# Optimization experiments

Measured on AMD Instinct MI355X. Metric: run time of the kernel, lower is better.

## Reference

```python
import jax, jax.numpy as jnp
import numpy as np

B, S, E, H = 2, 2048, 1024, 16
D = E // H  # head size

def setup_inputs() -> dict:
    key = jax.random.key(0)
    ks = jax.random.split(key, 11)
    s = 0.02
    return {
        "q": jax.random.normal(ks[0], (B, S, E), jnp.float32),
        "k": jax.random.normal(ks[1], (B, S, E), jnp.float32),
        "v": jax.random.normal(ks[2], (B, S, E), jnp.float32),
        "Wq": jax.random.normal(ks[3], (E, E), jnp.float32) * s,
        "bq": jax.random.normal(ks[4], (E,), jnp.float32) * s,
        "Wk": jax.random.normal(ks[5], (E, E), jnp.float32) * s,
        "bk": jax.random.normal(ks[6], (E,), jnp.float32) * s,
        "Wv": jax.random.normal(ks[7], (E, E), jnp.float32) * s,
        "bv": jax.random.normal(ks[8], (E,), jnp.float32) * s,
        "Wo": jax.random.normal(ks[9], (E, E), jnp.float32) * s,
        "bo": jax.random.normal(ks[10], (E,), jnp.float32) * s,
    }

def reference(q, k, v, Wq, bq, Wk, bk, Wv, bv, Wo, bo):
    b, sq, _ = q.shape
    sk = k.shape[1]
    # linear projections, split into heads: [B,S,H,D]
    qh = (q @ Wq.T + bq).reshape(b, sq, H, D)
    kh = (k @ Wk.T + bk).reshape(b, sk, H, D)
    vh = (v @ Wv.T + bv).reshape(b, sk, H, D)
    # NOTE: original module does NOT scale by 1/sqrt(D)
    scores = jnp.einsum('bqhe,bkhe->bhqk', qh, kh)
    probs = jax.nn.softmax(scores, axis=-1)  # dropout = identity (eval)
    attn = jnp.einsum('bhqk,bkhe->bqhe', probs, vh).reshape(b, sq, E)
    return attn @ Wo.T + bo
```

## Files before the change

kernel.cpp:

```cpp
#include <hip/hip_runtime.h>
#include <stdint.h>

#define BH 2
#define SEQ 2048
#define EMB 1024
#define NH 16
#define HD 64
#define MROWS (BH * SEQ)
#define BHN (BH * NH)
#define LOG2E 1.44269504f

typedef __attribute__((ext_vector_type(8))) short bf16x8;
typedef __attribute__((ext_vector_type(4))) float f32x4;

static __device__ __forceinline__ unsigned short f2bf(float x) {
  union { float f; unsigned int u; } a; a.f = x;
  unsigned int r = a.u + 0x7fffu + ((a.u >> 16) & 1u);
  return (unsigned short)(r >> 16);
}

static __device__ __forceinline__ unsigned int cvtpk(float lo, float hi) {
  unsigned int r;
  asm("v_cvt_pk_bf16_f32 %0, %1, %2" : "=v"(r) : "v"(lo), "v"(hi));
  return r;
}

static __device__ __forceinline__ float vexp2(float x) {
  float r;
  asm("v_exp_f32 %0, %1" : "=v"(r) : "v"(x));
  return r;
}

struct Conv7 { const float* s[7]; unsigned short* d[7]; };

__global__ __launch_bounds__(256) void conv_all(Conv7 a) {
  const int b = blockIdx.x;
  int r, off;
  if (b < 12288) { r = b >> 12; off = b & 4095; }
  else { int t = b - 12288; r = 3 + (t >> 10); off = t & 1023; }
  const int i = (off * 256 + threadIdx.x) * 4;
  float4 v = *(const float4*)(a.s[r] + i);
  ushort4 o;
  o.x = f2bf(v.x); o.y = f2bf(v.y); o.z = f2bf(v.z); o.w = f2bf(v.w);
  *(ushort4*)(a.d[r] + i) = o;
}

struct B3 { const float* p[3]; };
struct Out3 { void* p[3]; };

template <int MODE>
__global__ __launch_bounds__(256) void gemm128(const unsigned short* __restrict__ Abase,
                                               const unsigned short* __restrict__ Bbase,
                                               B3 biases, Out3 outs) {
  __shared__ unsigned short lA[128 * 64];
  __shared__ unsigned short lB[128 * 64];
  const int z = blockIdx.z;
  const unsigned short* A  = Abase + (size_t)z * MROWS * EMB;
  const unsigned short* Bt = Bbase + (size_t)z * EMB * EMB;
  const float* bias = biases.p[z];
  const int tid = threadIdx.x;
  const int lane = tid & 63;
  const int w = tid >> 6;
  const int row0 = blockIdx.x * 128;
  const int col0 = blockIdx.y * 128;
  const int wr = (w >> 1) * 64;
  const int wc = (w & 1) * 64;
  const int r16 = lane & 15;
  const int g = lane >> 4;

  const int s_rowoff = (lane >> 3);
  const int s_col = ((lane & 7) ^ s_rowoff) * 8;

  f32x4 acc[4][4] = {};

  for (int kt = 0; kt < EMB / 64; ++kt) {
    const int k0 = kt * 64;
    __syncthreads();
#pragma unroll
    for (int j = 0; j < 4; ++j) {
      const int chunk = w * 4 + j;
      const int row = chunk * 8 + s_rowoff;
      __builtin_amdgcn_global_load_lds(
          (const __attribute__((address_space(1))) void*)(A + (size_t)(row0 + row) * EMB + k0 + s_col),
          (__attribute__((address_space(3))) void*)(lA + chunk * 512), 16, 0, 0);
      __builtin_amdgcn_global_load_lds(
          (const __attribute__((address_space(1))) void*)(Bt + (size_t)(col0 + row) * EMB + k0 + s_col),
          (__attribute__((address_space(3))) void*)(lB + chunk * 512), 16, 0, 0);
    }
    __syncthreads();
#pragma unroll
    for (int kk = 0; kk < 2; ++kk) {
      bf16x8 a[4], b[4];
#pragma unroll
      for (int m = 0; m < 4; ++m) {
        const int row = wr + m * 16 + r16;
        a[m] = *(const bf16x8*)(lA + row * 64 + (((kk << 2) + g) ^ (r16 & 7)) * 8);
      }
#pragma unroll
      for (int n = 0; n < 4; ++n) {
        const int row = wc + n * 16 + r16;
        b[n] = *(const bf16x8*)(lB + row * 64 + (((kk << 2) + g) ^ (r16 & 7)) * 8);
      }
#pragma unroll
      for (int m = 0; m < 4; ++m)
#pragma unroll
        for (int n = 0; n < 4; ++n)
          acc[m][n] = __builtin_amdgcn_mfma_f32_16x16x32_bf16(a[m], b[n], acc[m][n], 0, 0, 0);
    }
  }

  const float scl = (MODE == 0 && z == 0) ? LOG2E : 1.0f;
#pragma unroll
  for (int m = 0; m < 4; ++m) {
#pragma unroll
    for (int n = 0; n < 4; ++n) {
      const int colg = col0 + wc + n * 16 + r16;
      const float bv = bias[colg];
      const int rowbase = row0 + wr + m * 16 + g * 4;
      if (MODE == 0 && z == 2) {
        const int b_ = rowbase >> 11, s_ = rowbase & 2047;
        const int h_ = colg >> 6, d_ = colg & 63;
        ushort4 pk;
        pk.x = f2bf(acc[m][n][0] + bv);
        pk.y = f2bf(acc[m][n][1] + bv);
        pk.z = f2bf(acc[m][n][2] + bv);
        pk.w = f2bf(acc[m][n][3] + bv);
        *(ushort4*)((unsigned short*)outs.p[2] +
                    ((size_t)(b_ * NH + h_) * HD + d_) * SEQ + s_) = pk;
      } else {
#pragma unroll
        for (int j = 0; j < 4; ++j) {
          const int rowg = rowbase + j;
          const float v = (acc[m][n][j] + bv) * scl;
          if (MODE == 0) {
            const int b_ = rowg >> 11, s_ = rowg & 2047;
            const int h_ = colg >> 6, d_ = colg & 63;
            ((unsigned short*)outs.p[z])
                [(((size_t)(b_ * NH + h_) * SEQ + s_) << 6) + d_] = f2bf(v);
          } else {
            ((float*)outs.p[0])[(size_t)rowg * EMB + colg] = v;
          }
        }
      }
    }
  }
}

__global__ __launch_bounds__(256) void attn_fwd(const unsigned short* __restrict__ Qh,
                                                const unsigned short* __restrict__ Kh,
                                                const unsigned short* __restrict__ Vt,
                                                unsigned short* __restrict__ ctx) {
  __shared__ unsigned short lK[64 * 72];
  __shared__ unsigned short lV[64 * 72];
  __shared__ unsigned short lP[4][2][16 * 72];
  const int tid = threadIdx.x;
  const int lane = tid & 63;
  const int w = tid >> 6;
  const int r16 = lane & 15;
  const int g = lane >> 4;
  const int wg = blockIdx.x;
  const int xcd = wg & 7;
  const int slot = wg >> 3;
  const int bh = xcd + 8 * (slot >> 4);
  const int qb = slot & 15;
  const size_t base = (size_t)bh * SEQ * HD;
  const unsigned short* Q = Qh + base;
  const unsigned short* K = Kh + base;
  const unsigned short* V = Vt + base;
  const int q0 = qb * 128 + w * 32;

  bf16x8 bq[2][2];
#pragma unroll
  for (int mi = 0; mi < 2; ++mi)
#pragma unroll
    for (int kk = 0; kk < 2; ++kk)
      bq[mi][kk] = *(const bf16x8*)(Q + (size_t)(q0 + mi * 16 + r16) * HD + kk * 32 + g * 8);

  f32x4 oacc[2][4] = {};
  float lsum[2] = {0.f, 0.f};

  const int sr = tid >> 2;
  const int sc = (tid & 3) * 16;

  uint4 kr0 = *(const uint4*)(K + (size_t)sr * HD + sc);
  uint4 kr1 = *(const uint4*)(K + (size_t)sr * HD + sc + 8);
  uint4 vr0 = *(const uint4*)(V + (size_t)sr * SEQ + sc);
  uint4 vr1 = *(const uint4*)(V + (size_t)sr * SEQ + sc + 8);

  for (int t = 0; t < SEQ / 64; ++t) {
    __syncthreads();
    *(uint4*)(lK + sr * 72 + sc)     = kr0;
    *(uint4*)(lK + sr * 72 + sc + 8) = kr1;
    *(uint4*)(lV + sr * 72 + sc)     = vr0;
    *(uint4*)(lV + sr * 72 + sc + 8) = vr1;
    __syncthreads();

    if (t < SEQ / 64 - 1) {
      const int kv1 = (t + 1) * 64;
      kr0 = *(const uint4*)(K + (size_t)(kv1 + sr) * HD + sc);
      kr1 = *(const uint4*)(K + (size_t)(kv1 + sr) * HD + sc + 8);
      vr0 = *(const uint4*)(V + (size_t)sr * SEQ + kv1 + sc);
      vr1 = *(const uint4*)(V + (size_t)sr * SEQ + kv1 + sc + 8);
    }

    f32x4 st[2][4] = {};
    __builtin_amdgcn_s_setprio(1);
#pragma unroll
    for (int kk = 0; kk < 2; ++kk) {
      bf16x8 ak[4];
#pragma unroll
      for (int n = 0; n < 4; ++n)
        ak[n] = *(const bf16x8*)(lK + (n * 16 + r16) * 72 + kk * 32 + g * 8);
#pragma unroll
      for (int mi = 0; mi < 2; ++mi)
#pragma unroll
        for (int n = 0; n < 4; ++n)
          st[mi][n] = __builtin_amdgcn_mfma_f32_16x16x32_bf16(ak[n], bq[mi][kk], st[mi][n], 0, 0, 0);
    }
    __builtin_amdgcn_s_setprio(0);

#pragma unroll
    for (int mi = 0; mi < 2; ++mi) {
      float ls = 0.f;
#pragma unroll
      for (int n = 0; n < 4; ++n) {
        float p0 = vexp2(st[mi][n][0]);
        float p1 = vexp2(st[mi][n][1]);
        float p2 = vexp2(st[mi][n][2]);
        float p3 = vexp2(st[mi][n][3]);
        ls += (p0 + p1) + (p2 + p3);
        uint2 pk;
        pk.x = cvtpk(p0, p1);
        pk.y = cvtpk(p2, p3);
        *(uint2*)(&lP[w][mi][r16 * 72 + n * 16 + g * 4]) = pk;
      }
      lsum[mi] += ls;
    }
    asm volatile("s_waitcnt lgkmcnt(0)" ::: "memory");
    __builtin_amdgcn_sched_barrier(0);

    __builtin_amdgcn_s_setprio(1);
#pragma unroll
    for (int kk = 0; kk < 2; ++kk) {
      bf16x8 bv[4];
#pragma unroll
      for (int nd = 0; nd < 4; ++nd)
        bv[nd] = *(const bf16x8*)(lV + (nd * 16 + r16) * 72 + kk * 32 + g * 8);
#pragma unroll
      for (int mi = 0; mi < 2; ++mi) {
        bf16x8 ap = *(const bf16x8*)(&lP[w][mi][r16 * 72 + kk * 32 + g * 8]);
#pragma unroll
        for (int nd = 0; nd < 4; ++nd)
          oacc[mi][nd] = __builtin_amdgcn_mfma_f32_16x16x32_bf16(ap, bv[nd], oacc[mi][nd], 0, 0, 0);
      }
    }
    __builtin_amdgcn_s_setprio(0);
  }

  float linv[2];
#pragma unroll
  for (int mi = 0; mi < 2; ++mi) {
    float v = lsum[mi];
    v += __shfl_xor(v, 16, 64);
    v += __shfl_xor(v, 32, 64);
    linv[mi] = 1.0f / v;
  }
  float rr[2][4];
#pragma unroll
  for (int mi = 0; mi < 2; ++mi)
#pragma unroll
    for (int j = 0; j < 4; ++j)
      rr[mi][j] = __shfl(linv[mi], g * 4 + j, 64);

  const int b_ = bh >> 4, h_ = bh & 15;
#pragma unroll
  for (int mi = 0; mi < 2; ++mi)
#pragma unroll
    for (int nd = 0; nd < 4; ++nd)
#pragma unroll
      for (int j = 0; j < 4; ++j) {
        const int srow = q0 + mi * 16 + g * 4 + j;
        const int col = h_ * 64 + nd * 16 + r16;
        ctx[((size_t)(b_ * SEQ + srow) << 10) + col] = f2bf(oacc[mi][nd][j] * rr[mi][j]);
      }
}

extern "C" void kernel_launch(void* const* d_in, const int* in_sizes, int n_in,
                              void* d_out, int out_size, void* d_ws, size_t ws_size,
                              hipStream_t stream) {
  const float* q  = (const float*)d_in[0];
  const float* k  = (const float*)d_in[1];
  const float* v  = (const float*)d_in[2];
  const float* Wq = (const float*)d_in[3];
  const float* bq = (const float*)d_in[4];
  const float* Wk = (const float*)d_in[5];
  const float* bk = (const float*)d_in[6];
  const float* Wv = (const float*)d_in[7];
  const float* bv = (const float*)d_in[8];
  const float* Wo = (const float*)d_in[9];
  const float* bo = (const float*)d_in[10];

  char* ws = (char*)d_ws;
  const size_t SZ_ACT = (size_t)MROWS * EMB * 2;
  const size_t SZ_W   = (size_t)EMB * EMB * 2;
  unsigned short* qb  = (unsigned short*)(ws);
  unsigned short* kb  = (unsigned short*)(ws + SZ_ACT);
  unsigned short* vb  = (unsigned short*)(ws + 2 * SZ_ACT);
  unsigned short* Wqb = (unsigned short*)(ws + 3 * SZ_ACT);
  unsigned short* Wob = (unsigned short*)(ws + 3 * SZ_ACT + 3 * SZ_W);
  unsigned short* Qh  = (unsigned short*)(ws + 3 * SZ_ACT + 4 * SZ_W);
  unsigned short* Kh  = (unsigned short*)(ws + 4 * SZ_ACT + 4 * SZ_W);
  unsigned short* Vt  = (unsigned short*)(ws + 5 * SZ_ACT + 4 * SZ_W);
  unsigned short* ctx = (unsigned short*)(ws + 6 * SZ_ACT + 4 * SZ_W);

  Conv7 ca;
  ca.s[0] = q;  ca.s[1] = k;  ca.s[2] = v;
  ca.s[3] = Wq; ca.s[4] = Wk; ca.s[5] = Wv; ca.s[6] = Wo;
  ca.d[0] = qb; ca.d[1] = kb; ca.d[2] = vb;
  ca.d[3] = Wqb; ca.d[4] = Wqb + EMB * EMB; ca.d[5] = Wqb + 2 * EMB * EMB; ca.d[6] = Wob;
  conv_all<<<16384, 256, 0, stream>>>(ca);

  B3 bqkv; bqkv.p[0] = bq; bqkv.p[1] = bk; bqkv.p[2] = bv;
  Out3 oqkv; oqkv.p[0] = (void*)Qh; oqkv.p[1] = (void*)Kh; oqkv.p[2] = (void*)Vt;
  gemm128<0><<<dim3(MROWS / 128, EMB / 128, 3), 256, 0, stream>>>(qb, Wqb, bqkv, oqkv);

  attn_fwd<<<512, 256, 0, stream>>>(Qh, Kh, Vt, ctx);

  B3 bout; bout.p[0] = bo; bout.p[1] = bo; bout.p[2] = bo;
  Out3 oout; oout.p[0] = d_out; oout.p[1] = d_out; oout.p[2] = d_out;
  gemm128<1><<<dim3(MROWS / 128, EMB / 128, 1), 256, 0, stream>>>(ctx, Wob, bout, oout);
}
```

Baseline: 238.6 us.

## Rewrite attention with 32x32 MFMA, register P via permlane swap, double-buffered LDS

The attention kernel switches from 16x16x32 to 32x32x16 MFMA tiles. The probability tile is rearranged in registers with v_permlane32_swap, so it no longer round-trips through LDS. K/V tiles are double-buffered in swizzled LDS, which leaves one barrier per iteration instead of two. The QKV projection GEMM epilogue now stages outputs through shared memory to emit coalesced 16-byte stores into the head-major and transposed-V layouts, at the cost of extra barriers and LDS traffic.

Result: faster. 231.0 us (-3.2%).

```diff
diff --git a/kernel.cpp b/kernel.cpp
--- a/kernel.cpp
+++ b/kernel.cpp
@@ -12,6 +12,7 @@
 
 typedef __attribute__((ext_vector_type(8))) short bf16x8;
 typedef __attribute__((ext_vector_type(4))) float f32x4;
+typedef __attribute__((ext_vector_type(16))) float f32x16;
 
 static __device__ __forceinline__ unsigned short f2bf(float x) {
   union { float f; unsigned int u; } a; a.f = x;
@@ -29,6 +30,10 @@
   float r;
   asm("v_exp_f32 %0, %1" : "=v"(r) : "v"(x));
   return r;
+}
+
+static __device__ __forceinline__ void plswap(unsigned int& a, unsigned int& b) {
+  asm volatile("v_permlane32_swap_b32 %0, %1" : "+v"(a), "+v"(b));
 }
 
 struct Conv7 { const float* s[7]; unsigned short* d[7]; };
@@ -52,8 +57,9 @@
 __global__ __launch_bounds__(256) void gemm128(const unsigned short* __restrict__ Abase,
                                                const unsigned short* __restrict__ Bbase,
                                                B3 biases, Out3 outs) {
-  __shared__ unsigned short lA[128 * 64];
-  __shared__ unsigned short lB[128 * 64];
+  __shared__ unsigned short lsm[128 * 128];
+  unsigned short* lA = lsm;
+  unsigned short* lB = lsm + 128 * 64;
   const int z = blockIdx.z;
   const unsigned short* A  = Abase + (size_t)z * MROWS * EMB;
   const unsigned short* Bt = Bbase + (size_t)z * EMB * EMB;
@@ -109,38 +115,84 @@
     }
   }
 
-  const float scl = (MODE == 0 && z == 0) ? LOG2E : 1.0f;
-#pragma unroll
-  for (int m = 0; m < 4; ++m) {
-#pragma unroll
-    for (int n = 0; n < 4; ++n) {
-      const int colg = col0 + wc + n * 16 + r16;
-      const float bv = bias[colg];
-      const int rowbase = row0 + wr + m * 16 + g * 4;
-      if (MODE == 0 && z == 2) {
-        const int b_ = rowbase >> 11, s_ = rowbase & 2047;
-        const int h_ = colg >> 6, d_ = colg & 63;
-        ushort4 pk;
-        pk.x = f2bf(acc[m][n][0] + bv);
-        pk.y = f2bf(acc[m][n][1] + bv);
-        pk.z = f2bf(acc[m][n][2] + bv);
-        pk.w = f2bf(acc[m][n][3] + bv);
-        *(ushort4*)((unsigned short*)outs.p[2] +
-                    ((size_t)(b_ * NH + h_) * HD + d_) * SEQ + s_) = pk;
-      } else {
+  if (MODE == 1) {
+#pragma unroll
+    for (int m = 0; m < 4; ++m)
+#pragma unroll
+      for (int n = 0; n < 4; ++n) {
+        const int colg = col0 + wc + n * 16 + r16;
+        const float bv = bias[colg];
 #pragma unroll
         for (int j = 0; j < 4; ++j) {
-          const int rowg = rowbase + j;
-          const float v = (acc[m][n][j] + bv) * scl;
-          if (MODE == 0) {
-            const int b_ = rowg >> 11, s_ = rowg & 2047;
-            const int h_ = colg >> 6, d_ = colg & 63;
-            ((unsigned short*)outs.p[z])
-                [(((size_t)(b_ * NH + h_) * SEQ + s_) << 6) + d_] = f2bf(v);
-          } else {
-            ((float*)outs.p[0])[(size_t)rowg * EMB + colg] = v;
-          }
+          const int rowg = row0 + wr + m * 16 + g * 4 + j;
+          ((float*)outs.p[0])[(size_t)rowg * EMB + colg] = acc[m][n][j] + bv;
         }
+      }
+  } else {
+    const int b_ = row0 >> 11;
+    const int s0 = row0 & 2047;
+    const int h0 = col0 >> 6;
+    const float scl = (z == 0) ? LOG2E : 1.0f;
+    if (z != 2) {
+#pragma unroll
+      for (int half = 0; half < 2; ++half) {
+        __syncthreads();
+        if ((w >> 1) == half) {
+#pragma unroll
+          for (int m = 0; m < 4; ++m)
+#pragma unroll
+            for (int n = 0; n < 4; ++n) {
+              const int cl = wc + n * 16 + r16;
+              const float bv = bias[col0 + cl];
+#pragma unroll
+              for (int j = 0; j < 4; ++j)
+                lsm[(m * 16 + g * 4 + j) * 136 + cl] = f2bf((acc[m][n][j] + bv) * scl);
+            }
+        }
+        __syncthreads();
+        const int rr_ = tid >> 2, q4 = tid & 3;
+        const int h_ = h0 + (q4 >> 1);
+        unsigned short* dst = (unsigned short*)outs.p[z] +
+            ((size_t)(b_ * NH + h_) * SEQ + s0 + half * 64 + rr_) * 64 + (q4 & 1) * 32;
+        uint4 x0 = *(uint4*)&lsm[rr_ * 136 + q4 * 32];
+        uint4 x1 = *(uint4*)&lsm[rr_ * 136 + q4 * 32 + 8];
+        uint4 x2 = *(uint4*)&lsm[rr_ * 136 + q4 * 32 + 16];
+        uint4 x3 = *(uint4*)&lsm[rr_ * 136 + q4 * 32 + 24];
+        *(uint4*)dst = x0;
+        *(uint4*)(dst + 8) = x1;
+        *(uint4*)(dst + 16) = x2;
+        *(uint4*)(dst + 24) = x3;
+      }
+    } else {
+#pragma unroll
+      for (int half = 0; half < 2; ++half) {
+        __syncthreads();
+        if ((w >> 1) == half) {
+#pragma unroll
+          for (int m = 0; m < 4; ++m)
+#pragma unroll
+            for (int n = 0; n < 4; ++n) {
+              const int cl = wc + n * 16 + r16;
+              const float bv = bias[col0 + cl];
+#pragma unroll
+              for (int j = 0; j < 4; ++j)
+                lsm[cl * 72 + m * 16 + g * 4 + j] = f2bf(acc[m][n][j] + bv);
+            }
+        }
+        __syncthreads();
+        const int c_ = tid >> 1, sh = tid & 1;
+        const int h_ = h0 + (c_ >> 6);
+        const int d_ = c_ & 63;
+        unsigned short* dst = (unsigned short*)outs.p[2] +
+            ((size_t)(b_ * NH + h_) * HD + d_) * SEQ + s0 + half * 64 + sh * 32;
+        uint4 y0 = *(uint4*)&lsm[c_ * 72 + sh * 32];
+        uint4 y1 = *(uint4*)&lsm[c_ * 72 + sh * 32 + 8];
+        uint4 y2 = *(uint4*)&lsm[c_ * 72 + sh * 32 + 16];
+        uint4 y3 = *(uint4*)&lsm[c_ * 72 + sh * 32 + 24];
+        *(uint4*)dst = y0;
+        *(uint4*)(dst + 8) = y1;
+        *(uint4*)(dst + 16) = y2;
+        *(uint4*)(dst + 24) = y3;
       }
     }
   }
@@ -150,14 +202,13 @@
                                                 const unsigned short* __restrict__ Kh,
                                                 const unsigned short* __restrict__ Vt,
                                                 unsigned short* __restrict__ ctx) {
-  __shared__ unsigned short lK[64 * 72];
-  __shared__ unsigned short lV[64 * 72];
-  __shared__ unsigned short lP[4][2][16 * 72];
+  __shared__ unsigned short kbuf[2][64 * 64];
+  __shared__ unsigned short vbuf[2][64 * 64];
   const int tid = threadIdx.x;
   const int lane = tid & 63;
   const int w = tid >> 6;
-  const int r16 = lane & 15;
-  const int g = lane >> 4;
+  const int l31 = lane & 31;
+  const int hi = lane >> 5;
   const int wg = blockIdx.x;
   const int xcd = wg & 7;
   const int slot = wg >> 3;
@@ -169,120 +220,103 @@
   const unsigned short* V = Vt + base;
   const int q0 = qb * 128 + w * 32;
 
-  bf16x8 bq[2][2];
-#pragma unroll
-  for (int mi = 0; mi < 2; ++mi)
-#pragma unroll
-    for (int kk = 0; kk < 2; ++kk)
-      bq[mi][kk] = *(const bf16x8*)(Q + (size_t)(q0 + mi * 16 + r16) * HD + kk * 32 + g * 8);
-
-  f32x4 oacc[2][4] = {};
-  float lsum[2] = {0.f, 0.f};
+  bf16x8 bq[4];
+#pragma unroll
+  for (int ks = 0; ks < 4; ++ks)
+    bq[ks] = *(const bf16x8*)(Q + (size_t)(q0 + l31) * HD + ks * 16 + hi * 8);
+
+  f32x16 oacc0 = {};
+  f32x16 oacc1 = {};
+  float lsum = 0.f;
 
   const int sr = tid >> 2;
-  const int sc = (tid & 3) * 16;
-
-  uint4 kr0 = *(const uint4*)(K + (size_t)sr * HD + sc);
-  uint4 kr1 = *(const uint4*)(K + (size_t)sr * HD + sc + 8);
-  uint4 vr0 = *(const uint4*)(V + (size_t)sr * SEQ + sc);
-  uint4 vr1 = *(const uint4*)(V + (size_t)sr * SEQ + sc + 8);
-
-  for (int t = 0; t < SEQ / 64; ++t) {
+  const int sx = (tid & 3) * 2;
+  const int sd0 = ((sx) ^ (sr & 7)) * 8;
+  const int sd1 = ((sx + 1) ^ (sr & 7)) * 8;
+
+  const int NT = SEQ / 64;
+  uint4 kr0, kr1, vr0, vr1;
+  kr0 = *(const uint4*)(K + (size_t)sr * HD + sx * 8);
+  kr1 = *(const uint4*)(K + (size_t)sr * HD + sx * 8 + 8);
+  vr0 = *(const uint4*)(V + (size_t)sr * SEQ + sx * 8);
+  vr1 = *(const uint4*)(V + (size_t)sr * SEQ + sx * 8 + 8);
+  *(uint4*)(kbuf[0] + sr * 64 + sd0) = kr0;
+  *(uint4*)(kbuf[0] + sr * 64 + sd1) = kr1;
+  *(uint4*)(vbuf[0] + sr * 64 + sd0) = vr0;
+  *(uint4*)(vbuf[0] + sr * 64 + sd1) = vr1;
+  kr0 = *(const uint4*)(K + (size_t)(64 + sr) * HD + sx * 8);
+  kr1 = *(const uint4*)(K + (size_t)(64 + sr) * HD + sx * 8 + 8);
+  vr0 = *(const uint4*)(V + (size_t)sr * SEQ + 64 + sx * 8);
+  vr1 = *(const uint4*)(V + (size_t)sr * SEQ + 64 + sx * 8 + 8);
+  __syncthreads();
+
+  for (int t = 0; t < NT; ++t) {
+    const unsigned short* lK = kbuf[t & 1];
+    const unsigned short* lV = vbuf[t & 1];
+#pragma unroll
+    for (int sub = 0; sub < 2; ++sub) {
+      f32x16 st = {};
+      __builtin_amdgcn_s_setprio(1);
+#pragma unroll
+      for (int ks = 0; ks < 4; ++ks) {
+        bf16x8 ak = *(const bf16x8*)(lK + (sub * 32 + l31) * 64 +
+                                     (((ks << 1) + hi) ^ (l31 & 7)) * 8);
+        st = __builtin_amdgcn_mfma_f32_32x32x16_bf16(ak, bq[ks], st, 0, 0, 0);
+      }
+      __builtin_amdgcn_s_setprio(0);
+      float p[16];
+#pragma unroll
+      for (int r = 0; r < 16; ++r) { p[r] = vexp2(st[r]); lsum += p[r]; }
+#pragma unroll
+      for (int h2 = 0; h2 < 2; ++h2) {
+        const int b8 = h2 * 8;
+        unsigned int a0 = cvtpk(p[b8 + 0], p[b8 + 1]);
+        unsigned int b0 = cvtpk(p[b8 + 4], p[b8 + 5]);
+        unsigned int a1 = cvtpk(p[b8 + 2], p[b8 + 3]);
+        unsigned int b1 = cvtpk(p[b8 + 6], p[b8 + 7]);
+        plswap(a0, b0);
+        plswap(a1, b1);
+        union { unsigned int u[4]; bf16x8 v; } pa;
+        pa.u[0] = a0; pa.u[1] = a1; pa.u[2] = b0; pa.u[3] = b1;
+        const int kst = sub * 2 + h2;
+        const int vsl = (((kst << 1) + hi) ^ (l31 & 7)) * 8;
+        bf16x8 v0 = *(const bf16x8*)(lV + l31 * 64 + vsl);
+        bf16x8 v1 = *(const bf16x8*)(lV + (32 + l31) * 64 + vsl);
+        __builtin_amdgcn_s_setprio(1);
+        oacc0 = __builtin_amdgcn_mfma_f32_32x32x16_bf16(pa.v, v0, oacc0, 0, 0, 0);
+        oacc1 = __builtin_amdgcn_mfma_f32_32x32x16_bf16(pa.v, v1, oacc1, 0, 0, 0);
+        __builtin_amdgcn_s_setprio(0);
+      }
+    }
+    if (t + 1 < NT) {
+      unsigned short* nK = kbuf[(t + 1) & 1];
+      unsigned short* nV = vbuf[(t + 1) & 1];
+      *(uint4*)(nK + sr * 64 + sd0) = kr0;
+      *(uint4*)(nK + sr * 64 + sd1) = kr1;
+      *(uint4*)(nV + sr * 64 + sd0) = vr0;
+      *(uint4*)(nV + sr * 64 + sd1) = vr1;
+      if (t + 2 < NT) {
+        const int kv2 = (t + 2) * 64;
+        kr0 = *(const uint4*)(K + (size_t)(kv2 + sr) * HD + sx * 8);
+        kr1 = *(const uint4*)(K + (size_t)(kv2 + sr) * HD + sx * 8 + 8);
+        vr0 = *(const uint4*)(V + (size_t)sr * SEQ + kv2 + sx * 8);
+        vr1 = *(const uint4*)(V + (size_t)sr * SEQ + kv2 + sx * 8 + 8);
+      }
+    }
     __syncthreads();
-    *(uint4*)(lK + sr * 72 + sc)     = kr0;
-    *(uint4*)(lK + sr * 72 + sc + 8) = kr1;
-    *(uint4*)(lV + sr * 72 + sc)     = vr0;
-    *(uint4*)(lV + sr * 72 + sc + 8) = vr1;
-    __syncthreads();
-
-    if (t < SEQ / 64 - 1) {
-      const int kv1 = (t + 1) * 64;
-      kr0 = *(const uint4*)(K + (size_t)(kv1 + sr) * HD + sc);
-      kr1 = *(const uint4*)(K + (size_t)(kv1 + sr) * HD + sc + 8);
-      vr0 = *(const uint4*)(V + (size_t)sr * SEQ + kv1 + sc);
-      vr1 = *(const uint4*)(V + (size_t)sr * SEQ + kv1 + sc + 8);
-    }
-
-    f32x4 st[2][4] = {};
-    __builtin_amdgcn_s_setprio(1);
-#pragma unroll
-    for (int kk = 0; kk < 2; ++kk) {
-      bf16x8 ak[4];
-#pragma unroll
-      for (int n = 0; n < 4; ++n)
-        ak[n] = *(const bf16x8*)(lK + (n * 16 + r16) * 72 + kk * 32 + g * 8);
-#pragma unroll
-      for (int mi = 0; mi < 2; ++mi)
-#pragma unroll
-        for (int n = 0; n < 4; ++n)
-          st[mi][n] = __builtin_amdgcn_mfma_f32_16x16x32_bf16(ak[n], bq[mi][kk], st[mi][n], 0, 0, 0);
-    }
-    __builtin_amdgcn_s_setprio(0);
-
-#pragma unroll
-    for (int mi = 0; mi < 2; ++mi) {
-      float ls = 0.f;
-#pragma unroll
-      for (int n = 0; n < 4; ++n) {
-        float p0 = vexp2(st[mi][n][0]);
-        float p1 = vexp2(st[mi][n][1]);
-        float p2 = vexp2(st[mi][n][2]);
-        float p3 = vexp2(st[mi][n][3]);
-        ls += (p0 + p1) + (p2 + p3);
-        uint2 pk;
-        pk.x = cvtpk(p0, p1);
-        pk.y = cvtpk(p2, p3);
-        *(uint2*)(&lP[w][mi][r16 * 72 + n * 16 + g * 4]) = pk;
-      }
-      lsum[mi] += ls;
-    }
-    asm volatile("s_waitcnt lgkmcnt(0)" ::: "memory");
-    __builtin_amdgcn_sched_barrier(0);
-
-    __builtin_amdgcn_s_setprio(1);
-#pragma unroll
-    for (int kk = 0; kk < 2; ++kk) {
-      bf16x8 bv[4];
-#pragma unroll
-      for (int nd = 0; nd < 4; ++nd)
-        bv[nd] = *(const bf16x8*)(lV + (nd * 16 + r16) * 72 + kk * 32 + g * 8);
-#pragma unroll
-      for (int mi = 0; mi < 2; ++mi) {
-        bf16x8 ap = *(const bf16x8*)(&lP[w][mi][r16 * 72 + kk * 32 + g * 8]);
-#pragma unroll
-        for (int nd = 0; nd < 4; ++nd)
-          oacc[mi][nd] = __builtin_amdgcn_mfma_f32_16x16x32_bf16(ap, bv[nd], oacc[mi][nd], 0, 0, 0);
-      }
-    }
-    __builtin_amdgcn_s_setprio(0);
   }
 
-  float linv[2];
-#pragma unroll
-  for (int mi = 0; mi < 2; ++mi) {
-    float v = lsum[mi];
-    v += __shfl_xor(v, 16, 64);
-    v += __shfl_xor(v, 32, 64);
-    linv[mi] = 1.0f / v;
+  lsum += __shfl_xor(lsum, 32, 64);
+  const float linv = 1.0f / lsum;
+  const int b_ = bh >> 4, h_ = bh & 15;
+#pragma unroll
+  for (int reg = 0; reg < 16; ++reg) {
+    const int crow = (reg & 3) + 8 * (reg >> 2) + 4 * hi;
+    const float rv = __shfl(linv, crow, 64);
+    const size_t rowaddr = ((size_t)(b_ * SEQ + q0 + crow) << 10) + h_ * 64 + l31;
+    ctx[rowaddr]      = f2bf(oacc0[reg] * rv);
+    ctx[rowaddr + 32] = f2bf(oacc1[reg] * rv);
   }
-  float rr[2][4];
-#pragma unroll
-  for (int mi = 0; mi < 2; ++mi)
-#pragma unroll
-    for (int j = 0; j < 4; ++j)
-      rr[mi][j] = __shfl(linv[mi], g * 4 + j, 64);
-
-  const int b_ = bh >> 4, h_ = bh & 15;
-#pragma unroll
-  for (int mi = 0; mi < 2; ++mi)
-#pragma unroll
-    for (int nd = 0; nd < 4; ++nd)
-#pragma unroll
-      for (int j = 0; j < 4; ++j) {
-        const int srow = q0 + mi * 16 + g * 4 + j;
-        const int col = h_ * 64 + nd * 16 + r16;
-        ctx[((size_t)(b_ * SEQ + srow) << 10) + col] = f2bf(oacc[mi][nd][j] * rr[mi][j]);
-      }
 }
 
 extern "C" void kernel_launch(void* const* d_in, const int* in_sizes, int n_in,
```
